# Optimization experiments

Hardware: AMD Instinct MI355X
Metric: run time of the kernel (lower is better)

Reference implementation:

```python
import jax, jax.numpy as jnp
import numpy as np

H = W = 128  # render resolution (init height/width)
EPS = 1e-8

def _normalize(x, axis):
    return x / (jnp.linalg.norm(x, axis=axis, keepdims=True) + EPS)

def _render_one(pts, camrot, campos, proj, uv, faces):
    # pts (p,3), camrot (3,3), campos (3,), proj (3,1), uv (p,2), faces (f,3)
    pc = (pts - campos) @ camrot.T                       # camera-space verts (p,3)
    xy = pc[:, :2] * proj[:2, 0] / (pc[:, 2:3] + EPS)    # perspective projection -> NDC (p,2)
    v3d = pc[faces]                                      # (f,3,3)
    v2d = xy[faces]                                      # (f,3,2)
    n = jnp.cross(v3d[:, 1] - v3d[:, 0], v3d[:, 2] - v3d[:, 0])  # face normals (f,3)
    n1 = _normalize(n, axis=1)
    # pixel grid in NDC
    px = jnp.linspace(-1.0, 1.0, W)[None, None, :]
    py = jnp.linspace(1.0, -1.0, H)[None, :, None]
    ax, ay = v2d[:, 0, 0, None, None], v2d[:, 0, 1, None, None]
    bx, by = v2d[:, 1, 0, None, None], v2d[:, 1, 1, None, None]
    cx, cy = v2d[:, 2, 0, None, None], v2d[:, 2, 1, None, None]
    d = (by - cy) * (ax - cx) + (cx - bx) * (ay - cy)    # (f,1,1) signed 2*area
    l0 = ((by - cy) * (px - cx) + (cx - bx) * (py - cy)) / (d + EPS)
    l1 = ((cy - ay) * (px - cx) + (ax - cx) * (py - cy)) / (d + EPS)
    l2 = 1.0 - l0 - l1                                   # barycentrics (f,H,W)
    z = (l0 * v3d[:, 0, 2, None, None] + l1 * v3d[:, 1, 2, None, None]
         + l2 * v3d[:, 2, 2, None, None])                # interpolated depth (f,H,W)
    inside = (l0 >= 0) & (l1 >= 0) & (l2 >= 0) & (jnp.abs(d) > EPS) & (z > EPS)
    zm = jnp.where(inside, z, jnp.float32(1e10))
    idx = jnp.argmin(zm, axis=0)                         # nearest visible face per pixel (H,W)
    hard = jnp.any(inside, axis=0)[..., None].astype(pts.dtype)  # hardmask (H,W,1)
    take = lambda a: jnp.take_along_axis(a, idx[None], axis=0)[0]  # (H,W)
    uvsel = uv[faces][idx]                               # (H,W,3,2) per-pixel face uvs
    tc = (take(l0)[..., None] * uvsel[..., 0, :]
          + take(l1)[..., None] * uvsel[..., 1, :]
          + take(l2)[..., None] * uvsel[..., 2, :]) * hard  # imtexcoords (H,W,2)
    return tc, hard, n1

def _fragment_shader(tc, texture, mask):
    # nearest-filter texture lookup; texture (3,th,tw)
    th, tw = texture.shape[1], texture.shape[2]
    u = jnp.clip(tc[..., 0], 0.0, 1.0)
    v = jnp.clip(tc[..., 1], 0.0, 1.0)
    tx = jnp.round(u * (tw - 1)).astype(jnp.int32)
    ty = jnp.round((1.0 - v) * (th - 1)).astype(jnp.int32)
    color = texture[:, ty, tx].transpose(1, 2, 0)        # (H,W,3)
    return color * mask

def setup_inputs() -> dict:
    key = jax.random.key(0)
    ks = jax.random.split(key, 6)
    b, p, f = 3, 768, 1024
    points = jax.random.normal(ks[0], (b, p, 3), jnp.float32) * 0.3
    faces = jax.random.randint(ks[1], (f, 3), 0, p)
    camera_rot = jnp.broadcast_to(jnp.eye(3, dtype=jnp.float32), (b, 3, 3))
    camera_pos = jnp.zeros((b, 3), jnp.float32).at[:, 2].set(-3.0)  # objects in front of camera
    camera_proj = jnp.ones((3, 1), jnp.float32)
    uv = jax.random.uniform(ks[2], (b, p, 2), jnp.float32)
    texture = jax.random.uniform(ks[3], (b, 3, 512, 512), jnp.float32)
    ts = jax.random.normal(ks[4], (b, 3), jnp.float32)
    return dict(points=points, camera_rot=camera_rot, camera_pos=camera_pos,
                camera_proj=camera_proj, uv=uv, texture=texture, ts=ts, faces=faces)

def reference(points, camera_rot, camera_pos, camera_proj, uv, texture, ts, faces):
    b = points.shape[0]
    render = jax.vmap(_render_one, in_axes=(0, 0, 0, None, 0, None))
    tcs, masks, normals = render(points, camera_rot, camera_pos, camera_proj, uv, faces)
    ims = jax.vmap(_fragment_shader)(tcs, texture, masks)   # (b,H,W,3)
    probs = masks                                            # improb proxy == hardmask
    order = jnp.argsort(-ts[:, 2])                           # far -> near compositing order
    ims_s, probs_s, masks_s = ims[order], probs[order], masks[order]
    imrender, improb, fg = ims_s[0], probs_s[0], masks_s[0]
    for i in range(1, b):                                    # fixed small layer count
        m = masks_s[i] > 0.5
        imrender = jnp.where(m, ims_s[i], imrender)
        improb = jnp.where(m, probs_s[i], improb)
        fg = jnp.where(m, masks_s[i], fg)
    return imrender[None], improb[None], normals, fg[None]
```

## Files before the change

kernel.cpp:

```cpp
#include <hip/hip_runtime.h>
#include <math.h>

#define B_ 3
#define P_ 768
#define F_ 1024
#define H_ 128
#define W_ 128
#define HW_ (H_*W_)
#define EPS_ 1e-8f
#define FPB_ 16

#define OFF_PROB   49152
#define OFF_NORM   65536
#define OFF_FG     74752


__global__ __launch_bounds__(256) void raster_fwd(
    const float* __restrict__ points,
    const float* __restrict__ camrot,
    const float* __restrict__ campos,
    const float* __restrict__ proj,
    const int*   __restrict__ faces,
    float4* __restrict__ faceE,
    const float* __restrict__ uv,
    unsigned long long* __restrict__ packed,
    float*  __restrict__ normals_out)
{
#pragma clang fp contract(off)
    int tid = threadIdx.x;
    int b   = blockIdx.x >> 6;

    __shared__ float sE0x[FPB_], sE0y[FPB_], sE1x[FPB_], sE1y[FPB_];
    __shared__ float sCx[FPB_],  sCy[FPB_],  sDen[FPB_];
    __shared__ float sZ0[FPB_],  sZ1[FPB_],  sZ2[FPB_];
    __shared__ int   sXlo[FPB_], sYlo[FPB_], sWX[FPB_], sN[FPB_];

    if (tid < FPB_) {
        int wid = blockIdx.x * FPB_ + tid;
        int f   = wid - b * F_;

        const float* R = camrot + b * 9;
        float cpx = campos[b*3+0], cpy = campos[b*3+1], cpz = campos[b*3+2];
        float pj0 = proj[0], pj1 = proj[1];

        int idx3[3];
        float pcx[3], pcy[3], pcz[3], sx[3], sy[3];
        for (int v = 0; v < 3; ++v) {
            int vi = faces[f*3 + v];
            idx3[v] = vi;
            const float* P = points + (b*P_ + vi) * 3;
            float vx = P[0] - cpx;
            float vy = P[1] - cpy;
            float vz = P[2] - cpz;
            float qx = (vx*R[0] + vy*R[1]) + vz*R[2];
            float qy = (vx*R[3] + vy*R[4]) + vz*R[5];
            float qz = (vx*R[6] + vy*R[7]) + vz*R[8];
            pcx[v] = qx; pcy[v] = qy; pcz[v] = qz;
            float dz = qz + EPS_;
            sx[v] = (qx * pj0) / dz;
            sy[v] = (qy * pj1) / dz;
        }

        float ax = sx[0], ay = sy[0];
        float bx = sx[1], by = sy[1];
        float cx = sx[2], cy = sy[2];

        float e0x = by - cy;
        float e0y = cx - bx;
        float e1x = cy - ay;
        float e1y = ax - cx;
        float d = e0x*(ax - cx) + e0y*(ay - cy);
        float denom = d + EPS_;
        bool valid = fabsf(d) > EPS_;

        float4* rec = faceE + wid * 4;
        rec[0] = make_float4(e0x, e0y, e1x, e1y);
        rec[1] = make_float4(cx, cy, denom, valid ? 1.0f : 0.0f);
        const float* uvb = uv + b * P_ * 2;
        rec[2] = make_float4(uvb[idx3[0]*2+0], uvb[idx3[0]*2+1],
                             uvb[idx3[1]*2+0], uvb[idx3[1]*2+1]);
        rec[3] = make_float4(uvb[idx3[2]*2+0], uvb[idx3[2]*2+1], 0.0f, 0.0f);

        float ux = pcx[1]-pcx[0], uy = pcy[1]-pcy[0], uz = pcz[1]-pcz[0];
        float wx = pcx[2]-pcx[0], wy = pcy[2]-pcy[0], wz = pcz[2]-pcz[0];
        float nx = fmaf(uy, wz, -(uz*wy));
        float ny = fmaf(uz, wx, -(ux*wz));
        float nz = fmaf(ux, wy, -(uy*wx));
        float nn = sqrtf((nx*nx + ny*ny) + nz*nz) + 1e-8f;
        normals_out[wid*3+0] = nx / nn;
        normals_out[wid*3+1] = ny / nn;
        normals_out[wid*3+2] = nz / nn;

        int N = 0, xlo = 0, ylo = 0, wX = 1;
        if (valid) {
            float gx0 = (ax + 1.0f) * 63.5f;
            float gx1 = (bx + 1.0f) * 63.5f;
            float gx2 = (cx + 1.0f) * 63.5f;
            float gy0 = (1.0f - ay) * 63.5f;
            float gy1 = (1.0f - by) * 63.5f;
            float gy2 = (1.0f - cy) * 63.5f;
            xlo = max(0,   (int)ceilf (fminf(fminf(gx0,gx1),gx2) - 1.0f));
            int xhi = min(127, (int)floorf(fmaxf(fmaxf(gx0,gx1),gx2) + 1.0f));
            ylo = max(0,   (int)ceilf (fminf(fminf(gy0,gy1),gy2) - 1.0f));
            int yhi = min(127, (int)floorf(fmaxf(fmaxf(gy0,gy1),gy2) + 1.0f));
            int wXl = xhi - xlo + 1;
            int wYl = yhi - ylo + 1;
            if (wXl > 0 && wYl > 0) { N = wXl * wYl; wX = wXl; }
        }
        sE0x[tid] = e0x; sE0y[tid] = e0y; sE1x[tid] = e1x; sE1y[tid] = e1y;
        sCx[tid]  = cx;  sCy[tid]  = cy;  sDen[tid] = denom;
        sZ0[tid]  = pcz[0]; sZ1[tid] = pcz[1]; sZ2[tid] = pcz[2];
        sXlo[tid] = xlo; sYlo[tid] = ylo; sWX[tid] = wX; sN[tid] = N;
    }
    __syncthreads();

    const double STEP = 2.0 / 127.0;
    unsigned long long* cells = packed + b * HW_;
    int fbase = (blockIdx.x & 63) * FPB_;

    for (int fl = 0; fl < FPB_; ++fl) {
        int N = sN[fl];
        if (tid >= N) continue;

        float e0x = sE0x[fl], e0y = sE0y[fl], e1x = sE1x[fl], e1y = sE1y[fl];
        float cx  = sCx[fl],  cy  = sCy[fl],  denom = sDen[fl];
        float z0  = sZ0[fl],  z1  = sZ1[fl],  z2 = sZ2[fl];
        int xlo = sXlo[fl], ylo = sYlo[fl];
        unsigned f = (unsigned)(fbase + fl);

        unsigned uwX = (unsigned)sWX[fl];
        unsigned q = 256u / uwX;
        unsigned r = 256u - q * uwX;
        unsigned yy = (unsigned)tid / uwX;
        unsigned xx = (unsigned)tid - yy * uwX;

        for (int i = tid; i < N; i += 256) {
            int X = xlo + (int)xx;
            int Y = ylo + (int)yy;
            float px = (float)(-1.0 + (double)X * STEP);
            float py = (float)( 1.0 - (double)Y * STEP);
            float dx = px - cx;
            float dy = py - cy;
            float n0 = e0x*dx + e0y*dy;
            float n1 = e1x*dx + e1y*dy;
            float l0 = n0 / denom;
            float l1 = n1 / denom;
            float l2 = 1.0f - l0 - l1;
            float zz = (l0*z0 + l1*z1) + l2*z2;
            if (l0 >= 0.0f && l1 >= 0.0f && l2 >= 0.0f && zz > EPS_) {
                unsigned long long pk =
                    ((unsigned long long)__float_as_uint(zz) << 32) | f;
                atomicMin(&cells[Y * W_ + X], pk);
            }
            xx += r; yy += q;
            if (xx >= uwX) { xx -= uwX; yy += 1; }
        }
    }
}

__global__ __launch_bounds__(64) void shade_composite(
    const float4* __restrict__ faceE,
    const float*  __restrict__ tex,
    const float*  __restrict__ ts,
    const unsigned long long* __restrict__ packed,
    float* __restrict__ out)
{
#pragma clang fp contract(off)
    int pix = blockIdx.x * 64 + threadIdx.x;
    int y = pix >> 7;
    int x = pix & (W_ - 1);

    const double STEP = 2.0 / 127.0;
    float px = (float)(-1.0 + (double)x * STEP);
    float py = (float)( 1.0 - (double)y * STEP);

    const unsigned MISS_BITS = __float_as_uint(1e10f);

    unsigned long long pka = packed[0 * HW_ + pix];
    unsigned long long pkb = packed[1 * HW_ + pix];
    unsigned long long pkc = packed[2 * HW_ + pix];

    float k0 = ts[0*3+2], k1 = ts[1*3+2], k2 = ts[2*3+2];
    int o0 = 0, o1 = 1, o2 = 2;
    if (k1 > k0) { int ti=o0; o0=o1; o1=ti; float tf=k0; k0=k1; k1=tf; }
    if (k2 > k1) { int ti=o1; o1=o2; o2=ti; float tf=k1; k1=k2; k2=tf; }
    if (k1 > k0) { int ti=o0; o0=o1; o1=ti; float tf=k0; k0=k1; k1=tf; }

    unsigned long long p0 = (o0 == 0) ? pka : ((o0 == 1) ? pkb : pkc);
    unsigned long long p1 = (o1 == 0) ? pka : ((o1 == 1) ? pkb : pkc);
    unsigned long long p2 = (o2 == 0) ? pka : ((o2 == 1) ? pkb : pkc);
    bool h1 = (unsigned)(p1 >> 32) < MISS_BITS;
    bool h2 = (unsigned)(p2 >> 32) < MISS_BITS;

    int w = o0; unsigned long long pkw = p0;
    if (h1) { w = o1; pkw = p1; }
    if (h2) { w = o2; pkw = p2; }
    bool hardw = (unsigned)(pkw >> 32) < MISS_BITS;

    float sr = 0.0f, sg = 0.0f, sb = 0.0f, sm = 0.0f;
    if (hardw) {
        int fi = (int)(unsigned)pkw;
        const float4* rec = faceE + (w * F_ + fi) * 4;
        float4 A  = rec[0];
        float4 Bv = rec[1];
        float4 Cv = rec[2];
        float4 Dv = rec[3];

        float dx = px - Bv.x;
        float dy = py - Bv.y;
        float n0 = A.x*dx + A.y*dy;
        float n1 = A.z*dx + A.w*dy;
        float l0 = n0 / Bv.z;
        float l1 = n1 / Bv.z;
        float l2 = 1.0f - l0 - l1;
        float tu = (l0*Cv.x + l1*Cv.z) + l2*Dv.x;
        float tv = (l0*Cv.y + l1*Cv.w) + l2*Dv.y;
        float uc = fminf(fmaxf(tu, 0.0f), 1.0f);
        float vc = fminf(fmaxf(tv, 0.0f), 1.0f);
        int txi = (int)rintf(uc * 511.0f);
        int tyi = (int)rintf((1.0f - vc) * 511.0f);

        const float* tb = tex + w * 3 * 262144;
        int o = tyi*512 + txi;
        sr = tb[0*262144 + o];
        sg = tb[1*262144 + o];
        sb = tb[2*262144 + o];
        sm = 1.0f;
    }

    out[pix*3+0] = sr;
    out[pix*3+1] = sg;
    out[pix*3+2] = sb;
    out[OFF_PROB + pix] = sm;
    out[OFF_FG   + pix] = sm;
}

extern "C" void kernel_launch(void* const* d_in, const int* in_sizes, int n_in,
                              void* d_out, int out_size, void* d_ws, size_t ws_size,
                              hipStream_t stream) {
    const float* points = (const float*)d_in[0];
    const float* camrot = (const float*)d_in[1];
    const float* campos = (const float*)d_in[2];
    const float* proj   = (const float*)d_in[3];
    const float* uv     = (const float*)d_in[4];
    const float* tex    = (const float*)d_in[5];
    const float* ts     = (const float*)d_in[6];
    const int*   faces  = (const int*)d_in[7];
    float* out = (float*)d_out;

    char* ws = (char*)d_ws;
    float4* faceE = (float4*)(ws);
    unsigned long long* packed = (unsigned long long*)(ws + 196608);


    raster_fwd<<<dim3(B_*F_/FPB_), dim3(256), 0, stream>>>(
        points, camrot, campos, proj, faces, faceE, uv,
        packed, out + OFF_NORM);
    shade_composite<<<dim3(HW_/64), dim3(64), 0, stream>>>(
        faceE, tex, ts, packed, out);
}
```

Before: 82.98 us.

## Parallelize vertex transform per vertex and assign faces to wavefronts

Face setup is split into two steps. First, 48 threads each transform and project one vertex and stage the results and its uv in shared memory. Then 16 threads assemble the edge, normal and bounding-box data from those staged values. The pixel loop now gives each 64-lane wavefront 4 faces to iterate over, instead of having all 256 threads sweep every face's bounding box in turn. This aims to cut the serial setup latency and the idle threads on small triangles. It adds an extra barrier, and load can become unbalanced across wavefronts when a few faces are large.

```diff
diff --git a/kernel.cpp b/kernel.cpp
--- a/kernel.cpp
+++ b/kernel.cpp
@@ -30,40 +30,50 @@
     int tid = threadIdx.x;
     int b   = blockIdx.x >> 6;
 
+    __shared__ float sV[FPB_*3][8];
     __shared__ float sE0x[FPB_], sE0y[FPB_], sE1x[FPB_], sE1y[FPB_];
     __shared__ float sCx[FPB_],  sCy[FPB_],  sDen[FPB_];
     __shared__ float sZ0[FPB_],  sZ1[FPB_],  sZ2[FPB_];
     __shared__ int   sXlo[FPB_], sYlo[FPB_], sWX[FPB_], sN[FPB_];
 
-    if (tid < FPB_) {
-        int wid = blockIdx.x * FPB_ + tid;
-        int f   = wid - b * F_;
+    if (tid < FPB_*3) {
+        int fl = tid / 3;
+        int v  = tid - fl*3;
+        int f  = (blockIdx.x & 63) * FPB_ + fl;
+        int vi = faces[f*3 + v];
 
         const float* R = camrot + b * 9;
         float cpx = campos[b*3+0], cpy = campos[b*3+1], cpz = campos[b*3+2];
         float pj0 = proj[0], pj1 = proj[1];
 
-        int idx3[3];
-        float pcx[3], pcy[3], pcz[3], sx[3], sy[3];
-        for (int v = 0; v < 3; ++v) {
-            int vi = faces[f*3 + v];
-            idx3[v] = vi;
-            const float* P = points + (b*P_ + vi) * 3;
-            float vx = P[0] - cpx;
-            float vy = P[1] - cpy;
-            float vz = P[2] - cpz;
-            float qx = (vx*R[0] + vy*R[1]) + vz*R[2];
-            float qy = (vx*R[3] + vy*R[4]) + vz*R[5];
-            float qz = (vx*R[6] + vy*R[7]) + vz*R[8];
-            pcx[v] = qx; pcy[v] = qy; pcz[v] = qz;
-            float dz = qz + EPS_;
-            sx[v] = (qx * pj0) / dz;
-            sy[v] = (qy * pj1) / dz;
-        }
-
-        float ax = sx[0], ay = sy[0];
-        float bx = sx[1], by = sy[1];
-        float cx = sx[2], cy = sy[2];
+        const float* P = points + (b*P_ + vi) * 3;
+        float vx = P[0] - cpx;
+        float vy = P[1] - cpy;
+        float vz = P[2] - cpz;
+        float qx = (vx*R[0] + vy*R[1]) + vz*R[2];
+        float qy = (vx*R[3] + vy*R[4]) + vz*R[5];
+        float qz = (vx*R[6] + vy*R[7]) + vz*R[8];
+        float dz = qz + EPS_;
+        float sxv = (qx * pj0) / dz;
+        float syv = (qy * pj1) / dz;
+
+        const float* uvb = uv + b * P_ * 2;
+        sV[tid][0] = qx;  sV[tid][1] = qy;  sV[tid][2] = qz;
+        sV[tid][3] = sxv; sV[tid][4] = syv;
+        sV[tid][5] = uvb[vi*2+0];
+        sV[tid][6] = uvb[vi*2+1];
+    }
+    __syncthreads();
+
+    if (tid < FPB_) {
+        int wid = blockIdx.x * FPB_ + tid;
+        const float* V0 = sV[tid*3+0];
+        const float* V1 = sV[tid*3+1];
+        const float* V2 = sV[tid*3+2];
+
+        float ax = V0[3], ay = V0[4];
+        float bx = V1[3], by = V1[4];
+        float cx = V2[3], cy = V2[4];
 
         float e0x = by - cy;
         float e0y = cx - bx;
@@ -76,13 +86,11 @@
         float4* rec = faceE + wid * 4;
         rec[0] = make_float4(e0x, e0y, e1x, e1y);
         rec[1] = make_float4(cx, cy, denom, valid ? 1.0f : 0.0f);
-        const float* uvb = uv + b * P_ * 2;
-        rec[2] = make_float4(uvb[idx3[0]*2+0], uvb[idx3[0]*2+1],
-                             uvb[idx3[1]*2+0], uvb[idx3[1]*2+1]);
-        rec[3] = make_float4(uvb[idx3[2]*2+0], uvb[idx3[2]*2+1], 0.0f, 0.0f);
-
-        float ux = pcx[1]-pcx[0], uy = pcy[1]-pcy[0], uz = pcz[1]-pcz[0];
-        float wx = pcx[2]-pcx[0], wy = pcy[2]-pcy[0], wz = pcz[2]-pcz[0];
+        rec[2] = make_float4(V0[5], V0[6], V1[5], V1[6]);
+        rec[3] = make_float4(V2[5], V2[6], 0.0f, 0.0f);
+
+        float ux = V1[0]-V0[0], uy = V1[1]-V0[1], uz = V1[2]-V0[2];
+        float wx = V2[0]-V0[0], wy = V2[1]-V0[1], wz = V2[2]-V0[2];
         float nx = fmaf(uy, wz, -(uz*wy));
         float ny = fmaf(uz, wx, -(ux*wz));
         float nz = fmaf(ux, wy, -(uy*wx));
@@ -109,7 +117,7 @@
         }
         sE0x[tid] = e0x; sE0y[tid] = e0y; sE1x[tid] = e1x; sE1y[tid] = e1y;
         sCx[tid]  = cx;  sCy[tid]  = cy;  sDen[tid] = denom;
-        sZ0[tid]  = pcz[0]; sZ1[tid] = pcz[1]; sZ2[tid] = pcz[2];
+        sZ0[tid]  = V0[2]; sZ1[tid] = V1[2]; sZ2[tid] = V2[2];
         sXlo[tid] = xlo; sYlo[tid] = ylo; sWX[tid] = wX; sN[tid] = N;
     }
     __syncthreads();
@@ -117,10 +125,13 @@
     const double STEP = 2.0 / 127.0;
     unsigned long long* cells = packed + b * HW_;
     int fbase = (blockIdx.x & 63) * FPB_;
-
-    for (int fl = 0; fl < FPB_; ++fl) {
+    int wv   = tid >> 6;
+    int lane = tid & 63;
+
+    for (int k = 0; k < 4; ++k) {
+        int fl = wv * 4 + k;
         int N = sN[fl];
-        if (tid >= N) continue;
+        if (lane >= N) continue;
 
         float e0x = sE0x[fl], e0y = sE0y[fl], e1x = sE1x[fl], e1y = sE1y[fl];
         float cx  = sCx[fl],  cy  = sCy[fl],  denom = sDen[fl];
@@ -129,12 +140,12 @@
         unsigned f = (unsigned)(fbase + fl);
 
         unsigned uwX = (unsigned)sWX[fl];
-        unsigned q = 256u / uwX;
-        unsigned r = 256u - q * uwX;
-        unsigned yy = (unsigned)tid / uwX;
-        unsigned xx = (unsigned)tid - yy * uwX;
-
-        for (int i = tid; i < N; i += 256) {
+        unsigned q = 64u / uwX;
+        unsigned r = 64u - q * uwX;
+        unsigned yy = (unsigned)lane / uwX;
+        unsigned xx = (unsigned)lane - yy * uwX;
+
+        for (int i = lane; i < N; i += 64) {
             int X = xlo + (int)xx;
             int Y = ylo + (int)yy;
             float px = (float)(-1.0 + (double)X * STEP);
```

Measured after the change: 83.34 us. Within noise of the previous version (+0.4%).
